# Optimization experiments

Measured on AMD Instinct MI355X. Metric: run time of the kernel, lower is better.

## Reference

```python
import jax, jax.numpy as jnp
import numpy as np

N_NODES = 100000
N_EDGES = 3200000


def spmm(row, col, val, h):
    # sparse [N,N] @ dense [N,D] via gather + segment_sum
    msg = val[:, None] * h[col]  # [E, D]
    return jax.ops.segment_sum(msg, row, num_segments=N_NODES)


def setup_inputs() -> dict:
    key = jax.random.key(0)
    k1, k2, k3, k4, k5, k6 = jax.random.split(key, 6)
    x = jax.random.normal(k1, (N_NODES, 512), dtype=jnp.float32)
    W1 = jax.random.normal(k2, (512, 64), dtype=jnp.float32) * 0.05
    W2 = jax.random.normal(k3, (64, 40), dtype=jnp.float32) * 0.1
    adj_val = jax.random.uniform(k4, (N_EDGES,), dtype=jnp.float32)
    adj_row = jax.random.randint(k5, (N_EDGES,), 0, N_NODES, dtype=jnp.int32)
    adj_col = jax.random.randint(k6, (N_EDGES,), 0, N_NODES, dtype=jnp.int32)
    return {"x": x, "W1": W1, "W2": W2, "adj_val": adj_val,
            "adj_row": adj_row, "adj_col": adj_col}


def reference(x, W1, W2, adj_val, adj_row, adj_col):
    # Layer 1: XW1, then A @ (XW1), relu
    h = x @ W1                              # [N, 64]
    h = spmm(adj_row, adj_col, adj_val, h)  # [N, 64]
    h = jax.nn.relu(h)
    # Layer 2: HW2, then A @ (HW2)
    h = h @ W2                              # [N, 40]
    out = spmm(adj_row, adj_col, adj_val, h)
    return out
```

## Files before the change

kernel.cpp:

```cpp
#include <hip/hip_runtime.h>

#define N_NODES 100000
#define N_EDGES 3200000
#define CH      12500
#define C_NB    256
#define NBUCK   782
#define G1_NB   1563

typedef unsigned int uint;
typedef unsigned short ushort;

typedef __attribute__((ext_vector_type(8))) short short8;
typedef __attribute__((ext_vector_type(4))) float floatx4;

static __device__ __forceinline__ ushort f2bf(float f) {
    uint u = __float_as_uint(f);
    u += 0x7fffu + ((u >> 16) & 1u);
    return (ushort)(u >> 16);
}
static __device__ __forceinline__ float bf2f(ushort h) {
    return __uint_as_float(((uint)h) << 16);
}

__global__ __launch_bounds__(256) void prep_kernel(const float* __restrict__ W1,
                                                   ushort* __restrict__ W1f,
                                                   int* __restrict__ cc) {
    if (blockIdx.x < 128) {
        int t = blockIdx.x * 256 + threadIdx.x;
        int j = t & 7;
        int lane = (t >> 3) & 63;
        int tile = t >> 9;
        int kt = tile >> 2, nt = tile & 3;
        int k = kt * 32 + ((lane >> 4) << 3) + j;
        int n = nt * 16 + (lane & 15);
        W1f[t] = f2bf(W1[k * 64 + n]);
    } else {
        int i = (blockIdx.x - 128) * 256 + threadIdx.x;
        if (i < NBUCK) cc[i] = 0;
    }
}

__global__ __launch_bounds__(256) void fused_g1_c1_kernel(const float* __restrict__ X,
                                                          const ushort* __restrict__ W1f,
                                                          ushort* __restrict__ H1,
                                                          const int* __restrict__ row,
                                                          int* __restrict__ cc,
                                                          int* __restrict__ blockbase) {
    __shared__ int hist[NBUCK];
    if (blockIdx.x < C_NB) {
        const int blk = blockIdx.x;
        for (int i = threadIdx.x; i < NBUCK; i += 256) hist[i] = 0;
        __syncthreads();
        const int4* rp = reinterpret_cast<const int4*>(row + (long)blk * CH);
        for (int i = threadIdx.x; i < CH / 4; i += 256) {
            int4 r = rp[i];
            atomicAdd(&hist[r.x >> 7], 1);
            atomicAdd(&hist[r.y >> 7], 1);
            atomicAdd(&hist[r.z >> 7], 1);
            atomicAdd(&hist[r.w >> 7], 1);
        }
        __syncthreads();
        for (int i = threadIdx.x; i < NBUCK; i += 256) {
            int c = hist[i];
            int base = 0;
            if (c) base = atomicAdd(&cc[i], c);
            blockbase[blk * NBUCK + i] = base;
        }
    } else {
        const int bid = blockIdx.x - C_NB;
        const int tid = threadIdx.x;
        const int wave = tid >> 6;
        const int lane = tid & 63;
        const int arow = bid * 64 + wave * 16 + (lane & 15);
        const bool valid = arow < N_NODES;
        const float* xr = X + (long)arow * 512 + ((lane >> 4) << 3);
        const short8* bb = reinterpret_cast<const short8*>(W1f) + lane;

        floatx4 acc0 = {0.f, 0.f, 0.f, 0.f};
        floatx4 acc1 = {0.f, 0.f, 0.f, 0.f};
        floatx4 acc2 = {0.f, 0.f, 0.f, 0.f};
        floatx4 acc3 = {0.f, 0.f, 0.f, 0.f};

        for (int kt = 0; kt < 16; ++kt) {
            float4 ax0, ax1;
            if (valid) {
                ax0 = *reinterpret_cast<const float4*>(xr + kt * 32);
                ax1 = *reinterpret_cast<const float4*>(xr + kt * 32 + 4);
            } else {
                ax0 = make_float4(0.f, 0.f, 0.f, 0.f);
                ax1 = ax0;
            }
            uint4 ap;
            ap.x = (__float_as_uint(ax0.x) >> 16) | (__float_as_uint(ax0.y) & 0xffff0000u);
            ap.y = (__float_as_uint(ax0.z) >> 16) | (__float_as_uint(ax0.w) & 0xffff0000u);
            ap.z = (__float_as_uint(ax1.x) >> 16) | (__float_as_uint(ax1.y) & 0xffff0000u);
            ap.w = (__float_as_uint(ax1.z) >> 16) | (__float_as_uint(ax1.w) & 0xffff0000u);
            short8 a = *reinterpret_cast<short8*>(&ap);

            const short8* bk = bb + kt * 4 * 64;
            acc0 = __builtin_amdgcn_mfma_f32_16x16x32_bf16(a, bk[0 * 64], acc0, 0, 0, 0);
            acc1 = __builtin_amdgcn_mfma_f32_16x16x32_bf16(a, bk[1 * 64], acc1, 0, 0, 0);
            acc2 = __builtin_amdgcn_mfma_f32_16x16x32_bf16(a, bk[2 * 64], acc2, 0, 0, 0);
            acc3 = __builtin_amdgcn_mfma_f32_16x16x32_bf16(a, bk[3 * 64], acc3, 0, 0, 0);
        }

        const int mrow = bid * 64 + wave * 16 + (lane >> 4) * 4;
        const int ncol = lane & 15;
        #pragma unroll
        for (int r = 0; r < 4; ++r) {
            int orow = mrow + r;
            if (orow < N_NODES) {
                ushort* o = H1 + (long)orow * 64 + ncol;
                o[0]  = f2bf(acc0[r]);
                o[16] = f2bf(acc1[r]);
                o[32] = f2bf(acc2[r]);
                o[48] = f2bf(acc3[r]);
            }
        }
    }
}

__global__ __launch_bounds__(1024) void c2_scan_kernel(const int* __restrict__ cc,
                                                       int* __restrict__ cptr) {
    __shared__ int sm[1024];
    const int tid = threadIdx.x;
    int v = (tid < NBUCK) ? cc[tid] : 0;
    sm[tid] = v;
    __syncthreads();
    #pragma unroll
    for (int off = 1; off < 1024; off <<= 1) {
        int t = (tid >= off) ? sm[tid - off] : 0;
        __syncthreads();
        sm[tid] += t;
        __syncthreads();
    }
    if (tid < NBUCK) cptr[tid] = sm[tid] - v;
    if (tid == NBUCK - 1) cptr[NBUCK] = sm[tid];
}

__global__ __launch_bounds__(256) void c3_kernel(const int* __restrict__ row,
                                                 const int* __restrict__ col,
                                                 const float* __restrict__ val,
                                                 const int* __restrict__ cptr,
                                                 const int* __restrict__ blockbase,
                                                 int2* __restrict__ staging) {
    __shared__ int cnt[NBUCK];
    const int blk = blockIdx.x;
    for (int i = threadIdx.x; i < NBUCK; i += 256) cnt[i] = 0;
    __syncthreads();
    const long e0 = (long)blk * CH;
    const int4* rp = reinterpret_cast<const int4*>(row + e0);
    const int4* cp = reinterpret_cast<const int4*>(col + e0);
    const int4* vp = reinterpret_cast<const int4*>(reinterpret_cast<const int*>(val) + e0);
    const int* bb = blockbase + blk * NBUCK;
    for (int i = threadIdx.x; i < CH / 4; i += 256) {
        int4 r = rp[i];
        int4 c = cp[i];
        int4 v = vp[i];
        #pragma unroll
        for (int q = 0; q < 4; ++q) {
            int rr = (q == 0) ? r.x : (q == 1) ? r.y : (q == 2) ? r.z : r.w;
            int ccol = (q == 0) ? c.x : (q == 1) ? c.y : (q == 2) ? c.z : c.w;
            int vv = (q == 0) ? v.x : (q == 1) ? v.y : (q == 2) ? v.z : v.w;
            int b = rr >> 7;
            int lr = atomicAdd(&cnt[b], 1);
            int slot = cptr[b] + bb[b] + lr;
            staging[slot] = make_int2((ccol << 7) | (rr & 127), vv);
        }
    }
}

__global__ __launch_bounds__(256) void c4_kernel(const int* __restrict__ cptr,
                                                 const int2* __restrict__ staging,
                                                 int2* __restrict__ edges,
                                                 int* __restrict__ rowptr) {
    __shared__ int cnt[128];
    __shared__ int sc[128];
    __shared__ int excl[129];
    __shared__ int cur[128];
    const int b = blockIdx.x;
    const int tid = threadIdx.x;
    const int lo = cptr[b], hi = cptr[b + 1];

    if (tid < 128) cnt[tid] = 0;
    __syncthreads();
    for (int i = lo + tid; i < hi; i += 256) atomicAdd(&cnt[staging[i].x & 127], 1);
    __syncthreads();
    if (tid < 128) sc[tid] = cnt[tid];
    __syncthreads();
    #pragma unroll
    for (int off = 1; off < 128; off <<= 1) {
        int t = 0;
        if (tid < 128 && tid >= off) t = sc[tid - off];
        __syncthreads();
        if (tid < 128) sc[tid] += t;
        __syncthreads();
    }
    if (tid < 128) {
        excl[tid] = sc[tid] - cnt[tid];
        cur[tid] = sc[tid] - cnt[tid];
    }
    if (tid == 127) excl[128] = sc[127];
    __syncthreads();
    if (tid <= 128) {
        int gr = b * 128 + tid;
        if (gr <= N_NODES) rowptr[gr] = lo + excl[tid];
    }
    __syncthreads();
    for (int i = lo + tid; i < hi; i += 256) {
        int2 ev = staging[i];
        int pos = atomicAdd(&cur[ev.x & 127], 1);
        edges[lo + pos] = make_int2(ev.x >> 7, ev.y);
    }
}

__global__ __launch_bounds__(256) void spmm1_w2_kernel(const int* __restrict__ rowptr,
                                                       const int2* __restrict__ edges,
                                                       const ushort* __restrict__ H1,
                                                       const float* __restrict__ W2,
                                                       ushort* __restrict__ H3) {
    __shared__ float Ws[64 * 40];
    __shared__ float hrow[4][64];
    for (int i = threadIdx.x; i < 64 * 40; i += 256) Ws[i] = W2[i];
    __syncthreads();

    const int r = blockIdx.x * 4 + (threadIdx.x >> 6);
    const int wave = threadIdx.x >> 6;
    const int lane = threadIdx.x & 63;
    if (r >= N_NODES) return;

    const int us = __builtin_amdgcn_readfirstlane(rowptr[r]);
    const int ue = __builtin_amdgcn_readfirstlane(rowptr[r + 1]);
    const int cnt = ue - us;
    const int2* __restrict__ ew = edges + us;

    float acc = 0.f;
    int j = 0;
    for (; j + 4 <= cnt; j += 4) {
        int2 e0 = ew[j + 0];
        int2 e1 = ew[j + 1];
        int2 e2 = ew[j + 2];
        int2 e3 = ew[j + 3];
        int o0 = e0.x * 64 + lane;
        int o1 = e1.x * 64 + lane;
        int o2 = e2.x * 64 + lane;
        int o3 = e3.x * 64 + lane;
        ushort h0 = H1[o0];
        ushort h1 = H1[o1];
        ushort h2 = H1[o2];
        ushort h3 = H1[o3];
        acc = fmaf(__int_as_float(e0.y), bf2f(h0), acc);
        acc = fmaf(__int_as_float(e1.y), bf2f(h1), acc);
        acc = fmaf(__int_as_float(e2.y), bf2f(h2), acc);
        acc = fmaf(__int_as_float(e3.y), bf2f(h3), acc);
    }
    for (; j < cnt; ++j) {
        int2 e = ew[j];
        acc = fmaf(__int_as_float(e.y), bf2f(H1[e.x * 64 + lane]), acc);
    }

    hrow[wave][lane] = fmaxf(acc, 0.f);
    float o = 0.f;
    if (lane < 40) {
        #pragma unroll
        for (int k = 0; k < 64; ++k) o += hrow[wave][k] * Ws[k * 40 + lane];
        H3[(long)r * 40 + lane] = f2bf(o);
    }
}

__global__ __launch_bounds__(256) void spmm2_kernel(const int* __restrict__ rowptr,
                                                    const int2* __restrict__ edges,
                                                    const ushort* __restrict__ H,
                                                    float* __restrict__ O) {
    const int r = blockIdx.x * 4 + (threadIdx.x >> 6);
    if (r >= N_NODES) return;
    const int lane = threadIdx.x & 63;

    const int us = __builtin_amdgcn_readfirstlane(rowptr[r]);
    const int ue = __builtin_amdgcn_readfirstlane(rowptr[r + 1]);
    const int cnt = ue - us;
    const int2* __restrict__ ew = edges + us;

    float acc = 0.f;
    int j = 0;
    for (; j + 4 <= cnt; j += 4) {
        int2 e0 = ew[j + 0];
        int2 e1 = ew[j + 1];
        int2 e2 = ew[j + 2];
        int2 e3 = ew[j + 3];
        int o0 = e0.x * 40 + lane;
        int o1 = e1.x * 40 + lane;
        int o2 = e2.x * 40 + lane;
        int o3 = e3.x * 40 + lane;
        ushort h0 = H[o0];
        ushort h1 = H[o1];
        ushort h2 = H[o2];
        ushort h3 = H[o3];
        acc = fmaf(__int_as_float(e0.y), bf2f(h0), acc);
        acc = fmaf(__int_as_float(e1.y), bf2f(h1), acc);
        acc = fmaf(__int_as_float(e2.y), bf2f(h2), acc);
        acc = fmaf(__int_as_float(e3.y), bf2f(h3), acc);
    }
    for (; j < cnt; ++j) {
        int2 e = ew[j];
        acc = fmaf(__int_as_float(e.y), bf2f(H[e.x * 40 + lane]), acc);
    }
    if (lane < 40) O[(long)r * 40 + lane] = acc;
}

extern "C" void kernel_launch(void* const* d_in, const int* in_sizes, int n_in,
                              void* d_out, int out_size, void* d_ws, size_t ws_size,
                              hipStream_t stream) {
    const float* x       = (const float*)d_in[0];
    const float* W1      = (const float*)d_in[1];
    const float* W2      = (const float*)d_in[2];
    const float* adj_val = (const float*)d_in[3];
    const int*   adj_row = (const int*)d_in[4];
    const int*   adj_col = (const int*)d_in[5];
    float* out = (float*)d_out;

    char* ws = (char*)d_ws;
    const size_t OFF_H1     = 0;
    const size_t OFF_STG    = 12800000;
    const size_t OFF_H3     = 12800000;
    const size_t OFF_EDGES  = 38400000;
    const size_t OFF_ROWPTR = 64000000;
    const size_t OFF_CC     = 64400016;
    const size_t OFF_CPTR   = 64403152;
    const size_t OFF_BB     = 64406288;
    const size_t OFF_W1F    = 65207056;

    ushort* h1     = (ushort*)(ws + OFF_H1);
    int2*   stg    = (int2*)(ws + OFF_STG);
    ushort* h3     = (ushort*)(ws + OFF_H3);
    int2*   edges  = (int2*)(ws + OFF_EDGES);
    int*    rowptr = (int*)(ws + OFF_ROWPTR);
    int*    cc     = (int*)(ws + OFF_CC);
    int*    cptr   = (int*)(ws + OFF_CPTR);
    int*    bb     = (int*)(ws + OFF_BB);
    ushort* w1f    = (ushort*)(ws + OFF_W1F);

    prep_kernel<<<128 + 4, 256, 0, stream>>>(W1, w1f, cc);

    fused_g1_c1_kernel<<<C_NB + G1_NB, 256, 0, stream>>>(x, w1f, h1, adj_row, cc, bb);

    c2_scan_kernel<<<1, 1024, 0, stream>>>(cc, cptr);

    c3_kernel<<<C_NB, 256, 0, stream>>>(adj_row, adj_col, adj_val, cptr, bb, stg);

    c4_kernel<<<NBUCK, 256, 0, stream>>>(cptr, stg, edges, rowptr);

    spmm1_w2_kernel<<<(N_NODES + 3) / 4, 256, 0, stream>>>(rowptr, edges, h1, W2, h3);

    spmm2_kernel<<<(N_NODES + 3) / 4, 256, 0, stream>>>(rowptr, edges, h3, out);
}
```

Baseline: 338.5 us.

## Pad CSR rows to multiples of eight and software-pipeline edge loads

The CSR build now pads each row's edge list to a multiple of eight with zero-weight dummy edges, and gives each 128-row bucket a fixed padding region so the offsets stay consistent. Both SpMM kernels drop their scalar remainder loop and use an 8-wide unrolled loop that prefetches the next eight edge records while the current gathers and FMAs run, which increases memory-level parallelism. In exchange the kernels read extra padded edges (up to seven per row, gathering row 0), c4 writes more zeros, and the workspace grows.

```diff
diff --git a/kernel.cpp b/kernel.cpp
--- a/kernel.cpp
+++ b/kernel.cpp
@@ -6,6 +6,7 @@
 #define C_NB    256
 #define NBUCK   782
 #define G1_NB   1563
+#define BPAD    1024
 
 typedef unsigned int uint;
 typedef unsigned short ushort;
@@ -176,17 +177,20 @@
                                                  int* __restrict__ rowptr) {
     __shared__ int cnt[128];
     __shared__ int sc[128];
-    __shared__ int excl[129];
+    __shared__ int pexcl[129];
     __shared__ int cur[128];
     const int b = blockIdx.x;
     const int tid = threadIdx.x;
     const int lo = cptr[b], hi = cptr[b + 1];
+    const int base = lo + BPAD * b;
+    const int nextbase = hi + BPAD * (b + 1);
 
     if (tid < 128) cnt[tid] = 0;
     __syncthreads();
     for (int i = lo + tid; i < hi; i += 256) atomicAdd(&cnt[staging[i].x & 127], 1);
     __syncthreads();
-    if (tid < 128) sc[tid] = cnt[tid];
+    int pv = 0;
+    if (tid < 128) { pv = (cnt[tid] + 7) & ~7; sc[tid] = pv; }
     __syncthreads();
     #pragma unroll
     for (int off = 1; off < 128; off <<= 1) {
@@ -196,21 +200,24 @@
         if (tid < 128) sc[tid] += t;
         __syncthreads();
     }
+    if (tid < 128) { pexcl[tid] = sc[tid] - pv; cur[tid] = sc[tid] - pv; }
+    if (tid == 127) pexcl[128] = sc[127];
+    __syncthreads();
     if (tid < 128) {
-        excl[tid] = sc[tid] - cnt[tid];
-        cur[tid] = sc[tid] - cnt[tid];
-    }
-    if (tid == 127) excl[128] = sc[127];
-    __syncthreads();
-    if (tid <= 128) {
         int gr = b * 128 + tid;
-        if (gr <= N_NODES) rowptr[gr] = lo + excl[tid];
-    }
+        if (gr <= N_NODES) rowptr[gr] = base + pexcl[tid];
+    }
+    if (tid < 128) {
+        int s = base + pexcl[tid] + cnt[tid];
+        int e = base + pexcl[tid + 1];
+        for (int i = s; i < e; ++i) edges[i] = make_int2(0, 0);
+    }
+    for (int i = base + pexcl[128] + tid; i < nextbase; i += 256) edges[i] = make_int2(0, 0);
     __syncthreads();
     for (int i = lo + tid; i < hi; i += 256) {
         int2 ev = staging[i];
         int pos = atomicAdd(&cur[ev.x & 127], 1);
-        edges[lo + pos] = make_int2(ev.x >> 7, ev.y);
+        edges[base + pos] = make_int2(ev.x >> 7, ev.y);
     }
 }
 
@@ -231,32 +238,38 @@
 
     const int us = __builtin_amdgcn_readfirstlane(rowptr[r]);
     const int ue = __builtin_amdgcn_readfirstlane(rowptr[r + 1]);
-    const int cnt = ue - us;
+    const int cnt8 = (ue - us) & ~7;
     const int2* __restrict__ ew = edges + us;
 
     float acc = 0.f;
-    int j = 0;
-    for (; j + 4 <= cnt; j += 4) {
-        int2 e0 = ew[j + 0];
-        int2 e1 = ew[j + 1];
-        int2 e2 = ew[j + 2];
-        int2 e3 = ew[j + 3];
-        int o0 = e0.x * 64 + lane;
-        int o1 = e1.x * 64 + lane;
-        int o2 = e2.x * 64 + lane;
-        int o3 = e3.x * 64 + lane;
-        ushort h0 = H1[o0];
-        ushort h1 = H1[o1];
-        ushort h2 = H1[o2];
-        ushort h3 = H1[o3];
-        acc = fmaf(__int_as_float(e0.y), bf2f(h0), acc);
-        acc = fmaf(__int_as_float(e1.y), bf2f(h1), acc);
-        acc = fmaf(__int_as_float(e2.y), bf2f(h2), acc);
-        acc = fmaf(__int_as_float(e3.y), bf2f(h3), acc);
-    }
-    for (; j < cnt; ++j) {
-        int2 e = ew[j];
-        acc = fmaf(__int_as_float(e.y), bf2f(H1[e.x * 64 + lane]), acc);
+    if (cnt8 > 0) {
+        int2 e0 = ew[0], e1 = ew[1], e2 = ew[2], e3 = ew[3];
+        int2 e4 = ew[4], e5 = ew[5], e6 = ew[6], e7 = ew[7];
+        int j = 8;
+        while (true) {
+            ushort h0 = H1[e0.x * 64 + lane];
+            ushort h1 = H1[e1.x * 64 + lane];
+            ushort h2 = H1[e2.x * 64 + lane];
+            ushort h3 = H1[e3.x * 64 + lane];
+            ushort h4 = H1[e4.x * 64 + lane];
+            ushort h5 = H1[e5.x * 64 + lane];
+            ushort h6 = H1[e6.x * 64 + lane];
+            ushort h7 = H1[e7.x * 64 + lane];
+            int2 n0 = ew[j + 0], n1 = ew[j + 1], n2 = ew[j + 2], n3 = ew[j + 3];
+            int2 n4 = ew[j + 4], n5 = ew[j + 5], n6 = ew[j + 6], n7 = ew[j + 7];
+            acc = fmaf(__int_as_float(e0.y), bf2f(h0), acc);
+            acc = fmaf(__int_as_float(e1.y), bf2f(h1), acc);
+            acc = fmaf(__int_as_float(e2.y), bf2f(h2), acc);
+            acc = fmaf(__int_as_float(e3.y), bf2f(h3), acc);
+            acc = fmaf(__int_as_float(e4.y), bf2f(h4), acc);
+            acc = fmaf(__int_as_float(e5.y), bf2f(h5), acc);
+            acc = fmaf(__int_as_float(e6.y), bf2f(h6), acc);
+            acc = fmaf(__int_as_float(e7.y), bf2f(h7), acc);
+            if (j >= cnt8) break;
+            e0 = n0; e1 = n1; e2 = n2; e3 = n3;
+            e4 = n4; e5 = n5; e6 = n6; e7 = n7;
+            j += 8;
+        }
     }
 
     hrow[wave][lane] = fmaxf(acc, 0.f);
@@ -278,32 +291,38 @@
 
     const int us = __builtin_amdgcn_readfirstlane(rowptr[r]);
     const int ue = __builtin_amdgcn_readfirstlane(rowptr[r + 1]);
-    const int cnt = ue - us;
+    const int cnt8 = (ue - us) & ~7;
     const int2* __restrict__ ew = edges + us;
 
     float acc = 0.f;
-    int j = 0;
-    for (; j + 4 <= cnt; j += 4) {
-        int2 e0 = ew[j + 0];
-        int2 e1 = ew[j + 1];
-        int2 e2 = ew[j + 2];
-        int2 e3 = ew[j + 3];
-        int o0 = e0.x * 40 + lane;
-        int o1 = e1.x * 40 + lane;
-        int o2 = e2.x * 40 + lane;
-        int o3 = e3.x * 40 + lane;
-        ushort h0 = H[o0];
-        ushort h1 = H[o1];
-        ushort h2 = H[o2];
-        ushort h3 = H[o3];
-        acc = fmaf(__int_as_float(e0.y), bf2f(h0), acc);
-        acc = fmaf(__int_as_float(e1.y), bf2f(h1), acc);
-        acc = fmaf(__int_as_float(e2.y), bf2f(h2), acc);
-        acc = fmaf(__int_as_float(e3.y), bf2f(h3), acc);
-    }
-    for (; j < cnt; ++j) {
-        int2 e = ew[j];
-        acc = fmaf(__int_as_float(e.y), bf2f(H[e.x * 40 + lane]), acc);
+    if (cnt8 > 0) {
+        int2 e0 = ew[0], e1 = ew[1], e2 = ew[2], e3 = ew[3];
+        int2 e4 = ew[4], e5 = ew[5], e6 = ew[6], e7 = ew[7];
+        int j = 8;
+        while (true) {
+            ushort h0 = H[e0.x * 40 + lane];
+            ushort h1 = H[e1.x * 40 + lane];
+            ushort h2 = H[e2.x * 40 + lane];
+            ushort h3 = H[e3.x * 40 + lane];
+            ushort h4 = H[e4.x * 40 + lane];
+            ushort h5 = H[e5.x * 40 + lane];
+            ushort h6 = H[e6.x * 40 + lane];
+            ushort h7 = H[e7.x * 40 + lane];
+            int2 n0 = ew[j + 0], n1 = ew[j + 1], n2 = ew[j + 2], n3 = ew[j + 3];
+            int2 n4 = ew[j + 4], n5 = ew[j + 5], n6 = ew[j + 6], n7 = ew[j + 7];
+            acc = fmaf(__int_as_float(e0.y), bf2f(h0), acc);
+            acc = fmaf(__int_as_float(e1.y), bf2f(h1), acc);
+            acc = fmaf(__int_as_float(e2.y), bf2f(h2), acc);
+            acc = fmaf(__int_as_float(e3.y), bf2f(h3), acc);
+            acc = fmaf(__int_as_float(e4.y), bf2f(h4), acc);
+            acc = fmaf(__int_as_float(e5.y), bf2f(h5), acc);
+            acc = fmaf(__int_as_float(e6.y), bf2f(h6), acc);
+            acc = fmaf(__int_as_float(e7.y), bf2f(h7), acc);
+            if (j >= cnt8) break;
+            e0 = n0; e1 = n1; e2 = n2; e3 = n3;
+            e4 = n4; e5 = n5; e6 = n6; e7 = n7;
+            j += 8;
+        }
     }
     if (lane < 40) O[(long)r * 40 + lane] = acc;
 }
@@ -324,11 +343,11 @@
     const size_t OFF_STG    = 12800000;
     const size_t OFF_H3     = 12800000;
     const size_t OFF_EDGES  = 38400000;
-    const size_t OFF_ROWPTR = 64000000;
-    const size_t OFF_CC     = 64400016;
-    const size_t OFF_CPTR   = 64403152;
-    const size_t OFF_BB     = 64406288;
-    const size_t OFF_W1F    = 65207056;
+    const size_t OFF_ROWPTR = 70406272;
+    const size_t OFF_CC     = 70806288;
+    const size_t OFF_CPTR   = 70809424;
+    const size_t OFF_BB     = 70812560;
+    const size_t OFF_W1F    = 71613328;
 
     ushort* h1     = (ushort*)(ws + OFF_H1);
     int2*   stg    = (int2*)(ws + OFF_STG);
```

New measurement: 723.6 us. +113.7%, slower.
